# Kernel tuning notes

Hardware: AMD Instinct MI355X
Metric: run time of the kernel (lower is better)

Reference implementation:

```python
import jax, jax.numpy as jnp
import numpy as np


def _ccl(x, w, b):
    # FFT-domain circular conv: rfft2 -> complex multiply + sum over c_in -> irfft2 + bias
    H, W = x.shape[-2], x.shape[-1]
    xf = jnp.fft.rfft2(x)                 # [B, Ci, H, Wf] complex
    wf = jnp.fft.rfft2(w, s=(H, W))       # [Co, Ci, H, Wf] complex
    hf = jnp.einsum('bihw,oihw->bohw', xf, wf)
    return jnp.fft.irfft2(hf, s=(H, W)) + b[:, None, None]


def _maxpool(x, ph, pw):
    B, C, H, W = x.shape
    return x.reshape(B, C, H // ph, ph, W // pw, pw).max(axis=(3, 5))


def _upsample_zero(x, sh, sw):
    B, C, H, W = x.shape
    y = jnp.zeros((B, C, H * sh, W * sw), dtype=x.dtype)
    return y.at[:, :, ::sh, ::sw].set(x)


def setup_inputs() -> dict:
    key = jax.random.key(0)
    ks = jax.random.split(key, 11)
    inp = {"x": jax.random.normal(ks[0], (16, 2, 64, 256), dtype=jnp.float32)}
    specs = [  # (c_out, c_in, kh, kw)
        (50, 1, 3, 7), (50, 50, 3, 7), (50, 50, 3, 5), (50, 50, 3, 7), (1, 50, 3, 7)]
    for i, (co, ci, kh, kw) in enumerate(specs):
        K = float(np.sqrt(1.0 / (ci * kh * kw)))
        inp[f"w{i+1}"] = (2 * jax.random.uniform(ks[2 * i + 1], (co, ci, kh, kw), dtype=jnp.float32) - 1) * K
        inp[f"b{i+1}"] = (2 * jax.random.uniform(ks[2 * i + 2], (co,), dtype=jnp.float32) - 1) * K
    return inp


def reference(x, w1, b1, w2, b2, w3, b3, w4, b4, w5, b5):
    H, W = x.shape[-2], x.shape[-1]
    h = x.reshape(-1, 1, H, W)                       # [2B, 1, 64, 256]
    h = jax.nn.relu(_maxpool(_ccl(h, w1, b1), 2, 4))  # [2B, 50, 32, 64]
    h = jax.nn.relu(_maxpool(_ccl(h, w2, b2), 2, 4))  # [2B, 50, 16, 16]
    h = h.reshape(-1, 2, h.shape[-3], h.shape[-2], h.shape[-1])
    h = h[:, 0] + h[:, 1].mean(axis=(-1, -2))[..., None, None]  # [B, 50, 16, 16]
    h = jax.nn.relu(_ccl(_upsample_zero(h, 2, 4), w3, b3))       # [B, 50, 32, 64]
    h = jax.nn.relu(_ccl(_upsample_zero(h, 2, 4), w4, b4))       # [B, 50, 64, 256]
    h = jax.nn.sigmoid(_ccl(h, w5, b5))                          # [B, 1, 64, 256]
    return h.squeeze(1)
```

## Files before the change

### kernel.cpp

```cpp
#include <hip/hip_runtime.h>
#include <math.h>

__global__ __launch_bounds__(256) void k1(const float* __restrict__ x,
                                          const float* __restrict__ w1,
                                          const float* __restrict__ b1,
                                          float* __restrict__ a1,
                                          const float* __restrict__ w2,
                                          const float* __restrict__ w3,
                                          const float* __restrict__ w4,
                                          float* __restrict__ w2t,
                                          float* __restrict__ w3t,
                                          float* __restrict__ w4t) {
  int b = blockIdx.z;
  int pr0 = blockIdx.x * 4;
  int co0 = blockIdx.y * 10;
  int ty = threadIdx.x >> 6;
  int pc = threadIdx.x & 63;
  int pr = pr0 + ty;
  const float* xb = x + b * (64 * 256);
  float xw[4][12];
#pragma unroll
  for (int r = 0; r < 4; ++r) {
    int row = (2 * pr - 2 + r) & 63;
    const float* rb = xb + row * 256;
#pragma unroll
    for (int v = 0; v < 3; ++v) {
      int col = (4 * pc - 8 + 4 * v) & 255;
      float4 t = *(const float4*)&rb[col];
      xw[r][4 * v + 0] = t.x; xw[r][4 * v + 1] = t.y;
      xw[r][4 * v + 2] = t.z; xw[r][4 * v + 3] = t.w;
    }
  }
#pragma unroll
  for (int cq = 0; cq < 10; ++cq) {
    int co = co0 + cq;
    const float* wp = w1 + co * 21;
    float m = -1e30f;
#pragma unroll
    for (int iy = 0; iy < 2; ++iy) {
#pragma unroll
      for (int jx = 0; jx < 4; ++jx) {
        float s = 0.f;
#pragma unroll
        for (int di = 0; di < 3; ++di)
#pragma unroll
          for (int dj = 0; dj < 7; ++dj)
            s = fmaf(xw[iy + 2 - di][jx + 8 - dj], wp[di * 7 + dj], s);
        m = fmaxf(m, s);
      }
    }
    float v = fmaxf(m + b1[co], 0.f);
    a1[((b * 50 + co) * 32 + pr) * 64 + pc] = v;
  }
  if (blockIdx.y == 0) {
    int base = (blockIdx.z * 8 + blockIdx.x) * 256 + threadIdx.x;
    for (int i = base; i < 90000; i += 65536) {
      if (i < 52500) {
        int co = i % 50, r = i / 50;
        w2t[i] = w2[co * 1050 + r];
        w4t[i] = w4[co * 1050 + r];
      } else {
        int j2 = i - 52500;
        int co = j2 % 50, r = j2 / 50;
        w3t[j2] = w3[co * 750 + r];
      }
    }
  }
}

__global__ __launch_bounds__(256) void k2(const float* __restrict__ a1,
                                          const float* __restrict__ w2t,
                                          const float* __restrict__ b2,
                                          float* __restrict__ a2) {
  __shared__ float sm[2560];
  int b = blockIdx.z;
  int r0 = blockIdx.x * 4;
  int co0 = blockIdx.y * 10;
  int y = threadIdx.x >> 6;
  int lane = threadIdx.x & 63;
  int offA = ((r0 + y - 2) & 31) * 64 + lane;
  int offB = ((r0 + y - 1) & 31) * 64 + lane;
  int offC = ((r0 + y) & 31) * 64 + lane;
  int idx1 = (lane - 1) & 63, idx2 = (lane - 2) & 63, idx3 = (lane - 3) & 63;
  int idx4 = (lane - 4) & 63, idx5 = (lane - 5) & 63, idx6 = (lane - 6) & 63;
  float acc[10];
#pragma unroll
  for (int co = 0; co < 10; ++co) acc[co] = b2[co0 + co];
  const float* ain = a1 + b * (50 * 2048);
  float vA = ain[offA], vB = ain[offB], vC = ain[offC];
  for (int ci = 0; ci < 50; ++ci) {
    int cin = (ci + 1 < 50) ? (ci + 1) : 49;
    const float* np = ain + cin * 2048;
    float nA = np[offA], nB = np[offB], nC = np[offC];
    const float* wci = w2t + ci * 1050 + co0;
#pragma unroll
    for (int di = 0; di < 3; ++di) {
      float v = (di == 0) ? vC : (di == 1) ? vB : vA;
      const float* wr = wci + di * 350;
      float x1 = __shfl(v, idx1, 64);
      float x2 = __shfl(v, idx2, 64);
      float x3 = __shfl(v, idx3, 64);
      float x4 = __shfl(v, idx4, 64);
      float x5 = __shfl(v, idx5, 64);
      float x6 = __shfl(v, idx6, 64);
#pragma unroll
      for (int co = 0; co < 10; ++co) acc[co] = fmaf(v,  wr[co], acc[co]);
#pragma unroll
      for (int co = 0; co < 10; ++co) acc[co] = fmaf(x1, wr[50 + co], acc[co]);
#pragma unroll
      for (int co = 0; co < 10; ++co) acc[co] = fmaf(x2, wr[100 + co], acc[co]);
#pragma unroll
      for (int co = 0; co < 10; ++co) acc[co] = fmaf(x3, wr[150 + co], acc[co]);
#pragma unroll
      for (int co = 0; co < 10; ++co) acc[co] = fmaf(x4, wr[200 + co], acc[co]);
#pragma unroll
      for (int co = 0; co < 10; ++co) acc[co] = fmaf(x5, wr[250 + co], acc[co]);
#pragma unroll
      for (int co = 0; co < 10; ++co) acc[co] = fmaf(x6, wr[300 + co], acc[co]);
    }
    vA = nA; vB = nB; vC = nC;
  }
#pragma unroll
  for (int k = 0; k < 10; ++k)
    sm[k * 256 + y * 64 + lane] = acc[k];
  __syncthreads();
  for (int w = threadIdx.x; w < 320; w += 256) {
    int cop = w / 32;
    int pr = (w >> 4) & 1;
    int pc = w & 15;
    float m = -1e30f;
#pragma unroll
    for (int yy = 0; yy < 2; ++yy)
#pragma unroll
      for (int xx = 0; xx < 4; ++xx)
        m = fmaxf(m, sm[cop * 256 + (pr * 2 + yy) * 64 + pc * 4 + xx]);
    m = fmaxf(m, 0.f);
    a2[((b * 50 + co0 + cop) * 16 + (r0 >> 1) + pr) * 16 + pc] = m;
  }
}

__global__ __launch_bounds__(512) void k3(const float* __restrict__ a2,
                                          const float* __restrict__ w3t,
                                          const float* __restrict__ b3,
                                          float* __restrict__ a3) {
  __shared__ float ts[4000];
  __shared__ float mean_s[64];
  __shared__ float part[200];
  int b = blockIdx.z;
  int r0 = blockIdx.x * 8;
  int co0 = blockIdx.y * 5;
  int tid = threadIdx.x;
  const float* aodd = a2 + (2 * b + 1) * (50 * 256);
  if (tid < 200) {
    int ci = tid >> 2, p = tid & 3;
    float s = 0.f;
    for (int k = 0; k < 64; ++k) s += aodd[ci * 256 + p * 64 + k];
    part[tid] = s;
  }
  __syncthreads();
  if (tid < 50)
    mean_s[tid] = (part[4 * tid] + part[4 * tid + 1] + part[4 * tid + 2] + part[4 * tid + 3]) * (1.f / 256.f);
  __syncthreads();
  const float* aev = a2 + (2 * b) * (50 * 256);
  for (int e = tid; e < 4000; e += 512) {
    int ci = e / 80;
    int rr = (e >> 4) % 5;
    int tc = e & 15;
    int trow = ((r0 >> 1) - 1 + rr) & 15;
    ts[e] = aev[ci * 256 + trow * 16 + tc] + mean_s[ci];
  }
  __syncthreads();
  int wv = __builtin_amdgcn_readfirstlane(tid >> 6);
  int lane = tid & 63;
  int p = wv >> 2;
  int m = wv & 3;
  int q = lane & 15;
  int yidx = lane >> 4;
  int i = r0 + 2 * yidx + p;
  int j = 4 * q + m;
  float acc[5];
#pragma unroll
  for (int co = 0; co < 5; ++co) acc[co] = b3[co0 + co];
  int ndi = (p == 0) ? 2 : 1;
  int ndj = (m == 0) ? 2 : 1;
  for (int aa = 0; aa < ndi; ++aa) {
    int di = (p == 0) ? (2 * aa) : 1;
    int rr = 1 + ((2 * yidx + p - di) >> 1);
    for (int e2 = 0; e2 < ndj; ++e2) {
      int dj = (m == 0) ? (4 * e2) : m;
      int tc = ((j - dj + 64) >> 2) & 15;
      for (int ci = 0; ci < 50; ++ci) {
        float xv = ts[ci * 80 + rr * 16 + tc];
        const float* wrow = w3t + (ci * 15 + di * 5 + dj) * 50 + co0;
#pragma unroll
        for (int co = 0; co < 5; ++co)
          acc[co] = fmaf(xv, wrow[co], acc[co]);
      }
    }
  }
  float* aout = a3 + b * (50 * 2048);
#pragma unroll
  for (int co = 0; co < 5; ++co)
    aout[(co0 + co) * 2048 + i * 64 + j] = fmaxf(acc[co], 0.f);
}

__global__ __launch_bounds__(512) void k4(const float* __restrict__ a3,
                                          const float* __restrict__ w4t,
                                          const float* __restrict__ b4,
                                          float* __restrict__ a4) {
  __shared__ __align__(16) float s4[9600];
  int b = blockIdx.z;
  int r0 = blockIdx.x * 4;
  int co0 = blockIdx.y * 10;
  int tid = threadIdx.x;
  const float* ain = a3 + b * (50 * 2048);
  int prb = (r0 >> 1) - 1;
  for (int e = tid; e < 2400; e += 512) {
    int ci = e / 48;
    int rem = e - ci * 48;
    int rr = rem >> 4;
    int c4 = rem & 15;
    int row = (prb + rr) & 31;
    *(float4*)&s4[(ci * 3 + rr) * 64 + c4 * 4] =
        *(const float4*)&ain[ci * 2048 + row * 64 + c4 * 4];
  }
  __syncthreads();
  int wv = __builtin_amdgcn_readfirstlane(tid >> 6);
  int lane = tid & 63;
  int rowsel = wv >> 2;
  int m = wv & 3;
  int j = 4 * lane + m;
  float acc[2][10];
#pragma unroll
  for (int co = 0; co < 10; ++co) {
    float bc = b4[co0 + co];
    acc[0][co] = bc; acc[1][co] = bc;
  }
  int ndi = (rowsel == 0) ? 2 : 1;
  int ndj = (m < 3) ? 2 : 1;
  for (int aa = 0; aa < ndi; ++aa) {
    int di = (rowsel == 0) ? (2 * aa) : 1;
    int rrb = 1 + ((rowsel - di) >> 1);
    for (int e2 = 0; e2 < ndj; ++e2) {
      int dj = m + 4 * e2;
      int tc = ((j - dj) >> 2) & 63;
      for (int ci = 0; ci < 50; ++ci) {
        float xv0 = s4[ci * 192 + rrb * 64 + tc];
        float xv1 = s4[ci * 192 + (rrb + 1) * 64 + tc];
        const float* wrow = w4t + (ci * 21 + di * 7 + dj) * 50 + co0;
#pragma unroll
        for (int co = 0; co < 10; ++co) {
          float w = wrow[co];
          acc[0][co] = fmaf(xv0, w, acc[0][co]);
          acc[1][co] = fmaf(xv1, w, acc[1][co]);
        }
      }
    }
  }
  float* aout = a4 + b * (50 * 16384);
  int i0 = r0 + rowsel, i1 = r0 + rowsel + 2;
#pragma unroll
  for (int co = 0; co < 10; ++co) {
    aout[(co0 + co) * 16384 + i0 * 256 + j] = fmaxf(acc[0][co], 0.f);
    aout[(co0 + co) * 16384 + i1 * 256 + j] = fmaxf(acc[1][co], 0.f);
  }
}

__global__ __launch_bounds__(512) void k5(const float* __restrict__ a4,
                                          const float* __restrict__ w5,
                                          const float* __restrict__ b5,
                                          float* __restrict__ out) {
  __shared__ __align__(16) float s5[4000];
  __shared__ float smw5[1056];
  int bid = blockIdx.x;
  int b = bid >> 5;
  int rem = bid & 31;
  int r0 = (rem >> 2) * 8;
  int jb = (rem & 3) * 64;
  int tid = threadIdx.x;
  int y = tid >> 6;
  int q = tid & 63;
  for (int e = tid; e < 1050; e += 512) smw5[e] = w5[e];
  float acc = b5[0];
  const float* ain = a4 + b * (50 * 16384);
  for (int cc = 0; cc < 10; ++cc) {
    __syncthreads();
    for (int e = tid; e < 1000; e += 512) {
      int ci = e / 200;
      int rem2 = e - ci * 200;
      int rr = rem2 / 20;
      int g = rem2 - rr * 20;
      int row = (r0 - 2 + rr) & 63;
      int col = (jb + 4 * g - 8) & 255;
      *(float4*)&s5[(ci * 10 + rr) * 80 + 4 * g] =
          *(const float4*)&ain[(cc * 5 + ci) * 16384 + row * 256 + col];
    }
    __syncthreads();
#pragma unroll
    for (int ci = 0; ci < 5; ++ci) {
#pragma unroll
      for (int di = 0; di < 3; ++di) {
        const float* base = s5 + ci * 800 + (y + 2 - di) * 80 + 8 + q;
        const float* wp = smw5 + ((cc * 5 + ci) * 3 + di) * 7;
#pragma unroll
        for (int dj = 0; dj < 7; ++dj)
          acc = fmaf(base[-dj], wp[dj], acc);
      }
    }
  }
  out[b * 16384 + (r0 + y) * 256 + jb + q] = 1.f / (1.f + expf(-acc));
}

extern "C" void kernel_launch(void* const* d_in, const int* in_sizes, int n_in,
                              void* d_out, int out_size, void* d_ws, size_t ws_size,
                              hipStream_t stream) {
  (void)in_sizes; (void)n_in; (void)out_size; (void)ws_size;
  const float* x  = (const float*)d_in[0];
  const float* w1 = (const float*)d_in[1];
  const float* b1 = (const float*)d_in[2];
  const float* w2 = (const float*)d_in[3];
  const float* b2 = (const float*)d_in[4];
  const float* w3 = (const float*)d_in[5];
  const float* b3 = (const float*)d_in[6];
  const float* w4 = (const float*)d_in[7];
  const float* b4 = (const float*)d_in[8];
  const float* w5 = (const float*)d_in[9];
  const float* b5 = (const float*)d_in[10];
  float* out = (float*)d_out;
  float* ws  = (float*)d_ws;
  float* w2t = ws;
  float* w3t = w2t + 52500;
  float* w4t = w3t + 37500;
  float* a1  = w4t + 52500;
  float* a2  = a1 + 32 * 50 * 32 * 64;
  float* a3  = a2 + 32 * 50 * 16 * 16;
  float* a4  = a3 + 16 * 50 * 32 * 64;
  hipLaunchKernelGGL(k1, dim3(8, 5, 32), dim3(256), 0, stream, x, w1, b1, a1,
                     w2, w3, w4, w2t, w3t, w4t);
  hipLaunchKernelGGL(k2, dim3(8, 5, 32), dim3(256), 0, stream, a1, w2t, b2, a2);
  hipLaunchKernelGGL(k3, dim3(4, 10, 16), dim3(512), 0, stream, a2, w3t, b3, a3);
  hipLaunchKernelGGL(k4, dim3(16, 5, 16), dim3(512), 0, stream, a3, w4t, b4, a4);
  hipLaunchKernelGGL(k5, dim3(512), dim3(512), 0, stream, a4, w5, b5, out);
}
```

Before: 302.2 us.

## Replace k4 shared-memory staging with register prefetch and wavefront shuffles

The k4 transposed-conv kernel no longer stages the input tile in LDS behind a block barrier. Each lane now loads its three input rows straight from global memory into registers, prefetching the next channel's values while computing the current one. The shifted-column neighbour comes from a cross-lane shuffle instead of an LDS read. This removes the LDS traffic and the barrier, but adds redundant global loads across waves and reorders the loops so the channel loop is outermost.

Measured after the change: 327.1 us. 1.08x slower.

```diff
diff --git a/kernel.cpp b/kernel.cpp
--- a/kernel.cpp
+++ b/kernel.cpp
@@ -208,54 +208,53 @@
                                           const float* __restrict__ w4t,
                                           const float* __restrict__ b4,
                                           float* __restrict__ a4) {
-  __shared__ __align__(16) float s4[9600];
   int b = blockIdx.z;
   int r0 = blockIdx.x * 4;
   int co0 = blockIdx.y * 10;
-  int tid = threadIdx.x;
-  const float* ain = a3 + b * (50 * 2048);
-  int prb = (r0 >> 1) - 1;
-  for (int e = tid; e < 2400; e += 512) {
-    int ci = e / 48;
-    int rem = e - ci * 48;
-    int rr = rem >> 4;
-    int c4 = rem & 15;
-    int row = (prb + rr) & 31;
-    *(float4*)&s4[(ci * 3 + rr) * 64 + c4 * 4] =
-        *(const float4*)&ain[ci * 2048 + row * 64 + c4 * 4];
-  }
-  __syncthreads();
-  int wv = __builtin_amdgcn_readfirstlane(tid >> 6);
-  int lane = tid & 63;
+  int wv = __builtin_amdgcn_readfirstlane(threadIdx.x >> 6);
+  int lane = threadIdx.x & 63;
   int rowsel = wv >> 2;
   int m = wv & 3;
   int j = 4 * lane + m;
+  int prb = (r0 >> 1) - 1;
+  int off0 = (prb & 31) * 64 + lane;
+  int off1 = ((prb + 1) & 31) * 64 + lane;
+  int off2 = ((prb + 2) & 31) * 64 + lane;
+  int idxm1 = (lane - 1) & 63;
   float acc[2][10];
 #pragma unroll
   for (int co = 0; co < 10; ++co) {
     float bc = b4[co0 + co];
     acc[0][co] = bc; acc[1][co] = bc;
   }
+  const float* ain = a3 + b * (50 * 2048);
+  float v0 = ain[off0], v1 = ain[off1], v2 = ain[off2];
   int ndi = (rowsel == 0) ? 2 : 1;
   int ndj = (m < 3) ? 2 : 1;
-  for (int aa = 0; aa < ndi; ++aa) {
-    int di = (rowsel == 0) ? (2 * aa) : 1;
-    int rrb = 1 + ((rowsel - di) >> 1);
-    for (int e2 = 0; e2 < ndj; ++e2) {
-      int dj = m + 4 * e2;
-      int tc = ((j - dj) >> 2) & 63;
-      for (int ci = 0; ci < 50; ++ci) {
-        float xv0 = s4[ci * 192 + rrb * 64 + tc];
-        float xv1 = s4[ci * 192 + (rrb + 1) * 64 + tc];
-        const float* wrow = w4t + (ci * 21 + di * 7 + dj) * 50 + co0;
+  for (int ci = 0; ci < 50; ++ci) {
+    int cin = (ci + 1 < 50) ? (ci + 1) : 49;
+    const float* np = ain + cin * 2048;
+    float n0 = np[off0], n1 = np[off1], n2 = np[off2];
+    const float* wci = w4t + ci * 21 * 50 + co0;
+    for (int aa = 0; aa < ndi; ++aa) {
+      int di = (rowsel == 0) ? (2 * aa) : 1;
+      int rrb = 1 + ((rowsel - di) >> 1);
+      float a0 = (rrb == 0) ? v0 : v1;
+      float a1 = (rrb == 0) ? v1 : v2;
+      for (int e2 = 0; e2 < ndj; ++e2) {
+        int dj = m + 4 * e2;
+        float x0 = (e2 == 0) ? a0 : __shfl(a0, idxm1, 64);
+        float x1 = (e2 == 0) ? a1 : __shfl(a1, idxm1, 64);
+        const float* wrow = wci + (di * 7 + dj) * 50;
 #pragma unroll
         for (int co = 0; co < 10; ++co) {
           float w = wrow[co];
-          acc[0][co] = fmaf(xv0, w, acc[0][co]);
-          acc[1][co] = fmaf(xv1, w, acc[1][co]);
+          acc[0][co] = fmaf(x0, w, acc[0][co]);
+          acc[1][co] = fmaf(x1, w, acc[1][co]);
         }
       }
     }
+    v0 = n0; v1 = n1; v2 = n2;
   }
   float* aout = a4 + b * (50 * 16384);
   int i0 = r0 + rowsel, i1 = r0 + rowsel + 2;
```
